# Kernel optimization log

Hardware: AMD Instinct MI355X
Metric: run time of the kernel (lower is better)

Reference implementation:

```python
import jax, jax.numpy as jnp
import numpy as np

E, H, FF = 1024, 16, 4096
HD = E // H
B, S = 4, 2048


def _ln(x, g, b, eps=1e-5):
    m = jnp.mean(x, axis=-1, keepdims=True)
    v = jnp.mean((x - m) ** 2, axis=-1, keepdims=True)
    return (x - m) / jnp.sqrt(v + eps) * g + b


def setup_inputs() -> dict:
    k = jax.random.key(0)
    ks = jax.random.split(k, 12)
    sd = 0.02
    return {
        "value": jax.random.normal(ks[0], (B, S, E), jnp.float32),
        "key": jax.random.normal(ks[1], (B, S, E), jnp.float32),
        "query": jax.random.normal(ks[2], (B, S, E), jnp.float32),
        "mask": jnp.ones((B, 1, 1, S), jnp.int32),
        "Wv": sd * jax.random.normal(ks[3], (E, E), jnp.float32),
        "Wk": sd * jax.random.normal(ks[4], (E, E), jnp.float32),
        "Wq": sd * jax.random.normal(ks[5], (E, E), jnp.float32),
        "Wo": sd * jax.random.normal(ks[6], (E, E), jnp.float32),
        "bo": jnp.zeros((E,), jnp.float32),
        "ln1_g": jnp.ones((E,), jnp.float32), "ln1_b": jnp.zeros((E,), jnp.float32),
        "ln2_g": jnp.ones((E,), jnp.float32), "ln2_b": jnp.zeros((E,), jnp.float32),
        "lnf_g": jnp.ones((E,), jnp.float32), "lnf_b": jnp.zeros((E,), jnp.float32),
        "W1": sd * jax.random.normal(ks[7], (E, FF), jnp.float32),
        "b1": jnp.zeros((FF,), jnp.float32),
        "W2": sd * jax.random.normal(ks[8], (FF, E), jnp.float32),
        "b2": jnp.zeros((E,), jnp.float32),
    }


def reference(value, key, query, mask, Wv, Wk, Wq, Wo, bo,
              ln1_g, ln1_b, ln2_g, ln2_b, lnf_g, lnf_b, W1, b1, W2, b2):
    N, Sq, Em = query.shape
    # pre-norms (value & key share prenorm2 params, as in the torch module)
    v = _ln(value, ln2_g, ln2_b)
    k = _ln(key, ln2_g, ln2_b)
    q = _ln(query, ln1_g, ln1_b)
    # QKV projections (no bias), split heads
    V = (v @ Wv).reshape(N, v.shape[1], H, HD)
    K = (k @ Wk).reshape(N, k.shape[1], H, HD)
    Q = (q @ Wq).reshape(N, Sq, H, HD)
    energy = jnp.einsum("nqhd,nkhd->nhqk", Q, K)  # [N,H,Sq,Sk]
    energy = jnp.where(mask == 0, jnp.float32(-1e20), energy)
    attn = jax.nn.softmax(energy / jnp.float32(HD ** 0.5), axis=-1)
    out = jnp.einsum("nhqk,nkhd->nqhd", attn, V).reshape(N, Sq, Em)
    out = out @ Wo + bo
    x = out + q  # residual (drop_path is identity in eval)
    f = _ln(x, lnf_g, lnf_b) @ W1 + b1
    f = jax.nn.gelu(f, approximate=False) @ W2 + b2
    return f + x
```

## Files before the change

kernel.cpp:

```cpp
#include <hip/hip_runtime.h>
#include <hip/hip_bf16.h>
#include <math.h>

typedef __bf16 bf16x8 __attribute__((ext_vector_type(8)));
typedef __bf16 bf16x4 __attribute__((ext_vector_type(4)));
typedef float f32x4 __attribute__((ext_vector_type(4)));
typedef float f32x2 __attribute__((ext_vector_type(2)));
typedef short s16x4 __attribute__((ext_vector_type(4)));

#define AS1 __attribute__((address_space(1)))
#define AS3 __attribute__((address_space(3)))

__device__ __forceinline__ void gll16(const __bf16* g, __bf16* l) {
    __builtin_amdgcn_global_load_lds((const AS1 unsigned int*)g,
                                     (AS3 unsigned int*)l, 16, 0, 0);
}

#if __has_builtin(__builtin_amdgcn_exp2f)
#define EXP2(x) __builtin_amdgcn_exp2f(x)
#else
#define EXP2(x) __expf((x) * 0.69314718055994530942f)
#endif

__device__ __forceinline__ f32x4 mfma16x16(bf16x4 a, bf16x4 b, f32x4 c) {
#if __has_builtin(__builtin_amdgcn_mfma_f32_16x16x16bf16_1k)
    union { bf16x4 h; s16x4 s; } ua, ub;
    ua.h = a; ub.h = b;
    return __builtin_amdgcn_mfma_f32_16x16x16bf16_1k(ua.s, ub.s, c, 0, 0, 0);
#else
    f32x4 d = c;
    asm volatile("v_mfma_f32_16x16x16_bf16 %0, %1, %2, %0"
                 : "+v"(d) : "v"(a), "v"(b));
    return d;
#endif
}

__global__ __launch_bounds__(256) void transpose_all(
    const float* __restrict__ Wq, const float* __restrict__ Wk,
    const float* __restrict__ Wv, const float* __restrict__ Wo,
    const float* __restrict__ W1, const float* __restrict__ W2,
    __bf16* __restrict__ Wqt, __bf16* __restrict__ Wkt,
    __bf16* __restrict__ Wvt, __bf16* __restrict__ Wot,
    __bf16* __restrict__ W1t, __bf16* __restrict__ W2t) {
    int g = blockIdx.x;
    const float* W; __bf16* Wt; int K, N, kt, nt;
    if (g < 4096) {
        int mi = g >> 10, loc = g & 1023;
        K = 1024; N = 1024; kt = loc >> 5; nt = loc & 31;
        W  = mi == 0 ? Wq  : mi == 1 ? Wk  : mi == 2 ? Wv  : Wo;
        Wt = mi == 0 ? Wqt : mi == 1 ? Wkt : mi == 2 ? Wvt : Wot;
    } else if (g < 8192) {
        int loc = g - 4096; W = W1; Wt = W1t;
        K = 1024; N = 4096; kt = loc >> 7; nt = loc & 127;
    } else {
        int loc = g - 8192; W = W2; Wt = W2t;
        K = 4096; N = 1024; kt = loc >> 5; nt = loc & 31;
    }
    int k0 = kt * 32, n0 = nt * 32;
    __shared__ float tile[32][33];
    int tx = threadIdx.x & 31, ty = threadIdx.x >> 5;
    #pragma unroll
    for (int j = ty; j < 32; j += 8)
        tile[j][tx] = W[(size_t)(k0 + j) * N + n0 + tx];
    __syncthreads();
    #pragma unroll
    for (int j = ty; j < 32; j += 8)
        Wt[(size_t)(n0 + j) * K + k0 + tx] = (__bf16)tile[tx][j];
}

__global__ __launch_bounds__(256) void ln3_kernel(
    const float* __restrict__ q, const float* __restrict__ k,
    const float* __restrict__ v,
    const float* __restrict__ g1, const float* __restrict__ b1,
    const float* __restrict__ g2, const float* __restrict__ b2,
    float* __restrict__ qln, __bf16* __restrict__ qbf,
    __bf16* __restrict__ kbf, __bf16* __restrict__ vbf) {
    const int E = 1024;
    int which = blockIdx.y;
    const float* x = which == 0 ? q : which == 1 ? k : v;
    const float* g = which == 0 ? g1 : g2;
    const float* bb = which == 0 ? b1 : b2;
    float* o32 = which == 0 ? qln : nullptr;
    __bf16* obf = which == 0 ? qbf : which == 1 ? kbf : vbf;

    size_t row = blockIdx.x;
    int t = threadIdx.x;
    float4 val = ((const float4*)(x + row * E))[t];
    float s  = val.x + val.y + val.z + val.w;
    float s2 = val.x * val.x + val.y * val.y + val.z * val.z + val.w * val.w;
    #pragma unroll
    for (int off = 32; off >= 1; off >>= 1) {
        s  += __shfl_down(s, off);
        s2 += __shfl_down(s2, off);
    }
    __shared__ float red[2][4];
    int wid = t >> 6, lane = t & 63;
    if (lane == 0) { red[0][wid] = s; red[1][wid] = s2; }
    __syncthreads();
    if (t == 0) {
        float S1 = red[0][0] + red[0][1] + red[0][2] + red[0][3];
        float S2 = red[1][0] + red[1][1] + red[1][2] + red[1][3];
        float mean = S1 / E;
        float var  = S2 / E - mean * mean;
        red[0][0] = mean;
        red[1][0] = 1.0f / sqrtf(var + 1e-5f);
    }
    __syncthreads();
    float mean = red[0][0], rstd = red[1][0];
    float4 gv = ((const float4*)g)[t];
    float4 bv = ((const float4*)bb)[t];
    float y0 = (val.x - mean) * rstd * gv.x + bv.x;
    float y1 = (val.y - mean) * rstd * gv.y + bv.y;
    float y2 = (val.z - mean) * rstd * gv.z + bv.z;
    float y3 = (val.w - mean) * rstd * gv.w + bv.w;
    if (o32) ((float4*)(o32 + row * E))[t] = make_float4(y0, y1, y2, y3);
    bf16x4 o;
    o[0] = (__bf16)y0; o[1] = (__bf16)y1; o[2] = (__bf16)y2; o[3] = (__bf16)y3;
    ((bf16x4*)(obf + row * E))[t] = o;
}

__global__ __launch_bounds__(256) void ln_kernel(const float* __restrict__ x,
                                                 const float* __restrict__ g,
                                                 const float* __restrict__ bb,
                                                 __bf16* __restrict__ outbf) {
    const int E = 1024;
    size_t row = blockIdx.x;
    int t = threadIdx.x;
    float4 v = ((const float4*)(x + row * E))[t];
    float s  = v.x + v.y + v.z + v.w;
    float s2 = v.x * v.x + v.y * v.y + v.z * v.z + v.w * v.w;
    #pragma unroll
    for (int off = 32; off >= 1; off >>= 1) {
        s  += __shfl_down(s, off);
        s2 += __shfl_down(s2, off);
    }
    __shared__ float red[2][4];
    int wid = t >> 6, lane = t & 63;
    if (lane == 0) { red[0][wid] = s; red[1][wid] = s2; }
    __syncthreads();
    if (t == 0) {
        float S1 = red[0][0] + red[0][1] + red[0][2] + red[0][3];
        float S2 = red[1][0] + red[1][1] + red[1][2] + red[1][3];
        float mean = S1 / E;
        float var  = S2 / E - mean * mean;
        red[0][0] = mean;
        red[1][0] = 1.0f / sqrtf(var + 1e-5f);
    }
    __syncthreads();
    float mean = red[0][0], rstd = red[1][0];
    float4 gv = ((const float4*)g)[t];
    float4 bv = ((const float4*)bb)[t];
    bf16x4 o;
    o[0] = (__bf16)((v.x - mean) * rstd * gv.x + bv.x);
    o[1] = (__bf16)((v.y - mean) * rstd * gv.y + bv.y);
    o[2] = (__bf16)((v.z - mean) * rstd * gv.z + bv.z);
    o[3] = (__bf16)((v.w - mean) * rstd * gv.w + bv.w);
    ((bf16x4*)(outbf + row * E))[t] = o;
}

template <int EPI>
__global__ __launch_bounds__(256) void gemm128(const __bf16* __restrict__ A,
                                               const __bf16* __restrict__ A2,
                                               const __bf16* __restrict__ Bt,
                                               const __bf16* __restrict__ Bt2,
                                               const float* __restrict__ bias,
                                               const float* __restrict__ resid,
                                               void* __restrict__ Cout,
                                               int M, int N, int K,
                                               int splitN, float scale) {
    __shared__ __bf16 As[128 * 64];
    __shared__ __bf16 Bs[128 * 64];
    int tid  = threadIdx.x;
    int lane = tid & 63, wid = tid >> 6;
    int quad = lane >> 4, l15 = lane & 15;
    int waveM = wid >> 1, waveN = wid & 1;

    int GX = N >> 7;
    int id = blockIdx.x;
    int x8 = id & 7, t = id >> 3;
    size_t rowBase = (size_t)((t / GX) * 8 + x8) * 128;
    size_t colBase = (size_t)(t % GX) * 128;

    const __bf16* Ap = A; const __bf16* Bp = Bt;
    size_t colLoc = colBase;
    float sc = scale;
    if ((int)colBase >= splitN) { Ap = A2; Bp = Bt2; colLoc = colBase - splitN; sc = 1.0f; }

    int lrow8  = lane >> 3;
    int lchunk = (lane & 7) ^ lrow8;
    const __bf16* Ag0 = Ap + (rowBase + wid * 32 + lrow8) * (size_t)K + lchunk * 8;
    const __bf16* Bg0 = Bp + (colLoc  + wid * 32 + lrow8) * (size_t)K + lchunk * 8;
    __bf16* AsB = &As[(wid * 32) * 64];
    __bf16* BsB = &Bs[(wid * 32) * 64];

    f32x4 acc[4][4] = {};
    int swz = l15 & 7;

    for (int kb = 0; kb < K; kb += 64) {
        __syncthreads();
        #pragma unroll
        for (int i = 0; i < 4; i++) {
            gll16(Ag0 + (size_t)i * 8 * K + kb, AsB + i * 512);
            gll16(Bg0 + (size_t)i * 8 * K + kb, BsB + i * 512);
        }
        __syncthreads();
        #pragma unroll
        for (int ks = 0; ks < 2; ks++) {
            int p = ((ks * 4 + quad) ^ swz) * 8;
            bf16x8 af[4], bfr[4];
            #pragma unroll
            for (int mi = 0; mi < 4; mi++)
                af[mi] = *(const bf16x8*)&As[(waveM * 64 + mi * 16 + l15) * 64 + p];
            #pragma unroll
            for (int ni = 0; ni < 4; ni++)
                bfr[ni] = *(const bf16x8*)&Bs[(waveN * 64 + ni * 16 + l15) * 64 + p];
            #pragma unroll
            for (int mi = 0; mi < 4; mi++)
                #pragma unroll
                for (int ni = 0; ni < 4; ni++)
                    acc[mi][ni] = __builtin_amdgcn_mfma_f32_16x16x32_bf16(
                        bfr[ni], af[mi], acc[mi][ni], 0, 0, 0);
        }
    }

    #pragma unroll
    for (int mi = 0; mi < 4; mi++)
    #pragma unroll
    for (int ni = 0; ni < 4; ni++) {
        size_t row = rowBase + waveM * 64 + mi * 16 + l15;
        size_t col = colBase + waveN * 64 + ni * 16 + quad * 4;
        f32x4 v = acc[mi][ni];
        if (EPI == 1) {
            float4 b4 = *(const float4*)&bias[col];
            float4 r4 = *(const float4*)&resid[row * N + col];
            float4 o;
            o.x = v[0] + b4.x + r4.x; o.y = v[1] + b4.y + r4.y;
            o.z = v[2] + b4.z + r4.z; o.w = v[3] + b4.w + r4.w;
            *(float4*)&((float*)Cout)[row * N + col] = o;
        } else if (EPI == 2) {
            float4 b4 = *(const float4*)&bias[col];
            bf16x4 pk;
            #pragma unroll
            for (int r = 0; r < 4; r++) {
                float t2 = v[r] + ((const float*)&b4)[r];
                pk[r] = (__bf16)(0.5f * t2 * (1.0f + erff(t2 * 0.70710678118654752f)));
            }
            *(bf16x4*)&((__bf16*)Cout)[row * N + col] = pk;
        } else {
            bf16x4 pk;
            #pragma unroll
            for (int r = 0; r < 4; r++) pk[r] = (__bf16)(v[r] * sc);
            *(bf16x4*)&((__bf16*)Cout)[row * N + col] = pk;
        }
    }
}

__global__ __launch_bounds__(256) void gemmV(const __bf16* __restrict__ A,
                                             const __bf16* __restrict__ Bt,
                                             __bf16* __restrict__ Cout,
                                             int M, int N, int K) {
    __shared__ __bf16 As[128 * 64];
    __shared__ __bf16 Bs[128 * 64];
    int tid  = threadIdx.x;
    int lane = tid & 63, wid = tid >> 6;
    int quad = lane >> 4, l15 = lane & 15;
    int waveM = wid >> 1, waveN = wid & 1;

    int GX = N >> 7;
    int id = blockIdx.x;
    int x8 = id & 7, t = id >> 3;
    size_t rowBase = (size_t)((t / GX) * 8 + x8) * 128;
    size_t colBase = (size_t)(t % GX) * 128;

    int lrow8  = lane >> 3;
    int lchunk = (lane & 7) ^ lrow8;
    const __bf16* Ag0 = A  + (rowBase + wid * 32 + lrow8) * (size_t)K + lchunk * 8;
    const __bf16* Bg0 = Bt + (colBase + wid * 32 + lrow8) * (size_t)K + lchunk * 8;
    __bf16* AsB = &As[(wid * 32) * 64];
    __bf16* BsB = &Bs[(wid * 32) * 64];

    f32x4 acc[4][4] = {};
    int swz = l15 & 7;

    for (int kb = 0; kb < K; kb += 64) {
        __syncthreads();
        #pragma unroll
        for (int i = 0; i < 4; i++) {
            gll16(Ag0 + (size_t)i * 8 * K + kb, AsB + i * 512);
            gll16(Bg0 + (size_t)i * 8 * K + kb, BsB + i * 512);
        }
        __syncthreads();
        #pragma unroll
        for (int ks = 0; ks < 2; ks++) {
            int p = ((ks * 4 + quad) ^ swz) * 8;
            bf16x8 af[4], bfr[4];
            #pragma unroll
            for (int mi = 0; mi < 4; mi++)
                af[mi] = *(const bf16x8*)&As[(waveM * 64 + mi * 16 + l15) * 64 + p];
            #pragma unroll
            for (int ni = 0; ni < 4; ni++)
                bfr[ni] = *(const bf16x8*)&Bs[(waveN * 64 + ni * 16 + l15) * 64 + p];
            #pragma unroll
            for (int mi = 0; mi < 4; mi++)
                #pragma unroll
                for (int ni = 0; ni < 4; ni++)
                    acc[mi][ni] = __builtin_amdgcn_mfma_f32_16x16x32_bf16(
                        af[mi], bfr[ni], acc[mi][ni], 0, 0, 0);
        }
    }

    #pragma unroll
    for (int mi = 0; mi < 4; mi++)
    #pragma unroll
    for (int ni = 0; ni < 4; ni++) {
        size_t col = colBase + waveN * 64 + ni * 16 + l15;
        size_t m0  = rowBase + waveM * 64 + mi * 16 + quad * 4;
        bf16x4 pk;
        #pragma unroll
        for (int r = 0; r < 4; r++) pk[r] = (__bf16)acc[mi][ni][r];
        *(bf16x4*)&Cout[col * M + m0] = pk;
    }
}

__global__ __launch_bounds__(512, 4) void attn_kernel(const __bf16* __restrict__ QK,
                                                      const __bf16* __restrict__ Vt,
                                                      const int* __restrict__ mask,
                                                      __bf16* __restrict__ Out) {
    const int S = 2048, E = 1024, E2 = 2048, M = 8192;
    int qt = blockIdx.x, bh = blockIdx.y;
    int b = bh >> 4, h = bh & 15;
    int q0 = qt * 256;
    int tid = threadIdx.x, lane = tid & 63, wid = tid >> 6;
    int quad = lane >> 4, l15 = lane & 15;

    __shared__ __bf16 Ks[2][4096];
    __shared__ __bf16 Vs[2][4096];

    bf16x8 aq[2][2];
    #pragma unroll
    for (int g = 0; g < 2; g++)
    #pragma unroll
    for (int hh = 0; hh < 2; hh++) {
        size_t row = (size_t)(b * S + q0 + wid * 32 + g * 16 + l15);
        aq[g][hh] = *(const bf16x8*)(QK + row * E2 + h * 64 + hh * 32 + quad * 8);
    }

    int lrow8  = lane >> 3;
    int lchunk = (lane & 7) ^ lrow8;
    const __bf16* Kg0 = QK + (size_t)(b * S + wid * 8 + lrow8) * E2 + 1024 + h * 64 + lchunk * 8;

    int rv = tid >> 3, cv = tid & 7;
    const __bf16* Vg0 = Vt + (size_t)(h * 64 + rv) * M + b * S + cv * 8;
    int c0   = ((cv & 1) << 2) + (cv >> 2);
    int lowb = (cv >> 1) & 1;
    int sv   = rv & 7;
    int wo0  = rv * 64 + ((c0 ^ sv) << 3) + (lowb << 2);
    int wo1  = rv * 64 + (((c0 + 2) ^ sv) << 3) + (lowb << 2);

    int swz = l15 & 7;

    f32x4 accO[2][4] = {};
    f32x2 acc2[2] = {};

    bf16x8 vreg = *(const bf16x8*)(Vg0);
    gll16(Kg0, &Ks[0][wid * 512]);
    *(bf16x4*)&Vs[0][wo0] = __builtin_shufflevector(vreg, vreg, 0, 1, 2, 3);
    *(bf16x4*)&Vs[0][wo1] = __builtin_shufflevector(vreg, vreg, 4, 5, 6, 7);
    __syncthreads();

    for (int kt = 0; kt < S / 64; kt++) {
        int k0 = kt * 64;
        int buf = kt & 1;
        if (kt + 1 < S / 64) {
            vreg = *(const bf16x8*)(Vg0 + k0 + 64);
            gll16(Kg0 + (size_t)(k0 + 64) * E2, &Ks[buf ^ 1][wid * 512]);
        }
        const __bf16* Ksb = &Ks[buf][0];
        const __bf16* Vsb = &Vs[buf][0];

        bf16x4 pb[2][4];
        #pragma unroll
        for (int nt = 0; nt < 4; nt++) {
            bf16x8 a0 = *(const bf16x8*)&Ksb[(nt * 16 + l15) * 64 + ((quad) ^ swz) * 8];
            bf16x8 a1 = *(const bf16x8*)&Ksb[(nt * 16 + l15) * 64 + ((4 + quad) ^ swz) * 8];
            int4 mz = *(const int4*)&mask[b * S + k0 + nt * 16 + quad * 4];
            #pragma unroll
            for (int g = 0; g < 2; g++) {
                f32x4 a = {};
                a = __builtin_amdgcn_mfma_f32_16x16x32_bf16(a0, aq[g][0], a, 0, 0, 0);
                a = __builtin_amdgcn_mfma_f32_16x16x32_bf16(a1, aq[g][1], a, 0, 0, 0);
                float p0 = mz.x ? EXP2(a[0]) : 0.f;
                float p1 = mz.y ? EXP2(a[1]) : 0.f;
                float p2 = mz.z ? EXP2(a[2]) : 0.f;
                float p3 = mz.w ? EXP2(a[3]) : 0.f;
                f32x2 t01; t01[0] = p0; t01[1] = p1;
                f32x2 t23; t23[0] = p2; t23[1] = p3;
                acc2[g] += t01 + t23;
                bf16x4 pk;
                pk[0] = (__bf16)p0; pk[1] = (__bf16)p1;
                pk[2] = (__bf16)p2; pk[3] = (__bf16)p3;
                pb[g][nt] = pk;
            }
        }

        #pragma unroll
        for (int dt = 0; dt < 4; dt++) {
            const __bf16* vrow = &Vsb[(dt * 16 + l15) * 64];
            bf16x8 vv0 = *(const bf16x8*)&vrow[((quad * 2 + 0) ^ swz) * 8];
            bf16x8 vv1 = *(const bf16x8*)&vrow[((quad * 2 + 1) ^ swz) * 8];
            bf16x4 h00 = __builtin_shufflevector(vv0, vv0, 0, 1, 2, 3);
            bf16x4 h01 = __builtin_shufflevector(vv0, vv0, 4, 5, 6, 7);
            bf16x4 h10 = __builtin_shufflevector(vv1, vv1, 0, 1, 2, 3);
            bf16x4 h11 = __builtin_shufflevector(vv1, vv1, 4, 5, 6, 7);
            #pragma unroll
            for (int g = 0; g < 2; g++) {
                accO[g][dt] = mfma16x16(h00, pb[g][0], accO[g][dt]);
                accO[g][dt] = mfma16x16(h01, pb[g][1], accO[g][dt]);
                accO[g][dt] = mfma16x16(h10, pb[g][2], accO[g][dt]);
                accO[g][dt] = mfma16x16(h11, pb[g][3], accO[g][dt]);
            }
        }

        if (kt + 1 < S / 64) {
            *(bf16x4*)&Vs[buf ^ 1][wo0] = __builtin_shufflevector(vreg, vreg, 0, 1, 2, 3);
            *(bf16x4*)&Vs[buf ^ 1][wo1] = __builtin_shufflevector(vreg, vreg, 4, 5, 6, 7);
        }
        __syncthreads();
    }

    #pragma unroll
    for (int g = 0; g < 2; g++) {
        float l = acc2[g][0] + acc2[g][1];
        l += __shfl_xor(l, 16, 64);
        l += __shfl_xor(l, 32, 64);
        float inv = 1.0f / l;
        #pragma unroll
        for (int dt = 0; dt < 4; dt++) {
            size_t row = (size_t)(b * S + q0 + wid * 32 + g * 16 + l15);
            bf16x4 pk;
            #pragma unroll
            for (int r = 0; r < 4; r++) pk[r] = (__bf16)(accO[g][dt][r] * inv);
            *(bf16x4*)&Out[row * E + h * 64 + dt * 16 + quad * 4] = pk;
        }
    }
}

extern "C" void kernel_launch(void* const* d_in, const int* in_sizes, int n_in,
                              void* d_out, int out_size, void* d_ws, size_t ws_size,
                              hipStream_t stream) {
    const int Bb = 4, S = 2048, E = 1024, FF = 4096;
    const int M = Bb * S;

    const float* value = (const float*)d_in[0];
    const float* key   = (const float*)d_in[1];
    const float* query = (const float*)d_in[2];
    const int*   mask  = (const int*)d_in[3];
    const float* Wv    = (const float*)d_in[4];
    const float* Wk    = (const float*)d_in[5];
    const float* Wq    = (const float*)d_in[6];
    const float* Wo    = (const float*)d_in[7];
    const float* bo    = (const float*)d_in[8];
    const float* ln1_g = (const float*)d_in[9];
    const float* ln1_b = (const float*)d_in[10];
    const float* ln2_g = (const float*)d_in[11];
    const float* ln2_b = (const float*)d_in[12];
    const float* lnf_g = (const float*)d_in[13];
    const float* lnf_b = (const float*)d_in[14];
    const float* W1    = (const float*)d_in[15];
    const float* b1    = (const float*)d_in[16];
    const float* W2    = (const float*)d_in[17];
    const float* b2    = (const float*)d_in[18];

    char* ws = (char*)d_ws;
    const size_t MB = 1024 * 1024;
    __bf16* Wqt = (__bf16*)(ws + 0 * MB);
    __bf16* Wkt = (__bf16*)(ws + 2 * MB);
    __bf16* Wvt = (__bf16*)(ws + 4 * MB);
    __bf16* Wot = (__bf16*)(ws + 6 * MB);
    __bf16* W1t = (__bf16*)(ws + 8 * MB);
    __bf16* W2t = (__bf16*)(ws + 16 * MB);
    __bf16* q_bf = (__bf16*)(ws + 24 * MB);
    __bf16* k_bf = (__bf16*)(ws + 40 * MB);
    __bf16* v_bf = (__bf16*)(ws + 56 * MB);
    __bf16* QKb  = (__bf16*)(ws + 72 * MB);
    __bf16* Vtg  = (__bf16*)(ws + 104 * MB);
    __bf16* attn = q_bf;
    __bf16* x_ln = k_bf;
    __bf16* h1   = v_bf;
    float*  qln  = (float*)(ws + 120 * MB);
    float*  x32  = (float*)(ws + 152 * MB);

    transpose_all<<<12288, 256, 0, stream>>>(Wq, Wk, Wv, Wo, W1, W2,
                                             Wqt, Wkt, Wvt, Wot, W1t, W2t);

    ln3_kernel<<<dim3(M, 3), 256, 0, stream>>>(query, key, value,
                                               ln1_g, ln1_b, ln2_g, ln2_b,
                                               qln, q_bf, k_bf, v_bf);

    gemm128<0><<<16 * 64, 256, 0, stream>>>(
        q_bf, k_bf, Wqt, Wkt, nullptr, nullptr, QKb, M, 2 * E, E, E,
        0.125f * 1.44269504088896f);

    gemmV<<<8 * 64, 256, 0, stream>>>(v_bf, Wvt, Vtg, M, E, E);

    attn_kernel<<<dim3(S / 256, Bb * 16), 512, 0, stream>>>(QKb, Vtg, mask, attn);

    gemm128<1><<<8 * 64, 256, 0, stream>>>(
        attn, attn, Wot, Wot, bo, qln, x32, M, E, E, E, 1.0f);

    ln_kernel<<<M, 256, 0, stream>>>(x32, lnf_g, lnf_b, x_ln);

    gemm128<2><<<32 * 64, 256, 0, stream>>>(
        x_ln, x_ln, W1t, W1t, b1, nullptr, h1, M, FF, E, FF, 1.0f);
    gemm128<1><<<8 * 64, 256, 0, stream>>>(
        h1, h1, W2t, W2t, b2, x32, (float*)d_out, M, E, FF, E, 1.0f);
}
```

Before: 652.9 us.

## Add 256x256 double-buffered GEMM kernel for QK projection and FFN1

Introduces a gemm256 kernel with 256x256 output tiles, 512 threads (8 waves), LDS double buffering via global_load_lds, and interleaved MFMA phases with s_setprio to overlap loads with compute. It replaces gemm128 for the fused Q/K projection and the W1+GELU GEMM. Larger tiles raise arithmetic intensity and cut global traffic per FLOP. In exchange, LDS use grows to 128KB per block and there are fewer blocks (256 for QK), which may underfill the CUs.

```diff
diff --git a/kernel.cpp b/kernel.cpp
--- a/kernel.cpp
+++ b/kernel.cpp
@@ -255,6 +255,168 @@
     }
 }
 
+template <int EPI>
+__global__ __launch_bounds__(512, 2) void gemm256(const __bf16* __restrict__ A,
+                                                  const __bf16* __restrict__ A2,
+                                                  const __bf16* __restrict__ Bt,
+                                                  const __bf16* __restrict__ Bt2,
+                                                  const float* __restrict__ bias,
+                                                  const float* __restrict__ resid,
+                                                  void* __restrict__ Cout,
+                                                  int M, int N, int K,
+                                                  int splitN, float scale) {
+    __shared__ __bf16 As[2][256 * 64];
+    __shared__ __bf16 Bs[2][256 * 64];
+    int tid  = threadIdx.x;
+    int lane = tid & 63, wid = tid >> 6;
+    int quad = lane >> 4, l15 = lane & 15;
+    int waveM = wid >> 2, waveN = wid & 3;
+
+    int GX = N >> 8;
+    int id = blockIdx.x;
+    int x8 = id & 7, tt = id >> 3;
+    size_t rowBase = (size_t)((tt / GX) * 8 + x8) * 256;
+    size_t colBase = (size_t)(tt % GX) * 256;
+
+    const __bf16* Ap = A; const __bf16* Bp = Bt;
+    size_t colLoc = colBase;
+    float sc = scale;
+    if ((int)colBase >= splitN) { Ap = A2; Bp = Bt2; colLoc = colBase - splitN; sc = 1.0f; }
+
+    int lrow8  = lane >> 3;
+    int lchunk = (lane & 7) ^ lrow8;
+    const __bf16* Ag0 = Ap + (rowBase + wid * 32 + lrow8) * (size_t)K + lchunk * 8;
+    const __bf16* Bg0 = Bp + (colLoc  + wid * 32 + lrow8) * (size_t)K + lchunk * 8;
+    int ldsB = (wid * 32) * 64;
+
+    f32x4 acc[8][4] = {};
+    int swz = l15 & 7;
+    int nsteps = K >> 6;
+
+    #pragma unroll
+    for (int i = 0; i < 4; i++) {
+        gll16(Ag0 + (size_t)i * 8 * K, &As[0][ldsB + i * 512]);
+        gll16(Bg0 + (size_t)i * 8 * K, &Bs[0][ldsB + i * 512]);
+    }
+    __syncthreads();
+
+    for (int t = 0; t < nsteps; t++) {
+        int cur = t & 1;
+        const __bf16* Asb = &As[cur][0];
+        const __bf16* Bsb = &Bs[cur][0];
+        __bf16* Asn = &As[cur ^ 1][0];
+        __bf16* Bsn = &Bs[cur ^ 1][0];
+        bool pre = (t + 1 < nsteps);
+        size_t kb = (size_t)(t + 1) << 6;
+
+        bf16x8 af[4], bfr[4];
+        int p0 = (quad ^ swz) * 8;
+        int p1 = ((4 + quad) ^ swz) * 8;
+
+        #pragma unroll
+        for (int ni = 0; ni < 4; ni++)
+            bfr[ni] = *(const bf16x8*)&Bsb[(waveN * 64 + ni * 16 + l15) * 64 + p0];
+        #pragma unroll
+        for (int mi = 0; mi < 4; mi++)
+            af[mi] = *(const bf16x8*)&Asb[(waveM * 128 + mi * 16 + l15) * 64 + p0];
+        if (pre) {
+            #pragma unroll
+            for (int i = 0; i < 4; i++)
+                gll16(Ag0 + (size_t)i * 8 * K + kb, &Asn[ldsB + i * 512]);
+        }
+        __builtin_amdgcn_s_barrier();
+        __builtin_amdgcn_s_setprio(1);
+        #pragma unroll
+        for (int mi = 0; mi < 4; mi++)
+            #pragma unroll
+            for (int ni = 0; ni < 4; ni++)
+                acc[mi][ni] = __builtin_amdgcn_mfma_f32_16x16x32_bf16(
+                    bfr[ni], af[mi], acc[mi][ni], 0, 0, 0);
+        __builtin_amdgcn_s_setprio(0);
+        __builtin_amdgcn_s_barrier();
+
+        #pragma unroll
+        for (int mi = 0; mi < 4; mi++)
+            af[mi] = *(const bf16x8*)&Asb[(waveM * 128 + (mi + 4) * 16 + l15) * 64 + p0];
+        if (pre) {
+            #pragma unroll
+            for (int i = 0; i < 4; i++)
+                gll16(Bg0 + (size_t)i * 8 * K + kb, &Bsn[ldsB + i * 512]);
+        }
+        __builtin_amdgcn_s_barrier();
+        __builtin_amdgcn_s_setprio(1);
+        #pragma unroll
+        for (int mi = 0; mi < 4; mi++)
+            #pragma unroll
+            for (int ni = 0; ni < 4; ni++)
+                acc[mi + 4][ni] = __builtin_amdgcn_mfma_f32_16x16x32_bf16(
+                    bfr[ni], af[mi], acc[mi + 4][ni], 0, 0, 0);
+        __builtin_amdgcn_s_setprio(0);
+        __builtin_amdgcn_s_barrier();
+
+        #pragma unroll
+        for (int ni = 0; ni < 4; ni++)
+            bfr[ni] = *(const bf16x8*)&Bsb[(waveN * 64 + ni * 16 + l15) * 64 + p1];
+        #pragma unroll
+        for (int mi = 0; mi < 4; mi++)
+            af[mi] = *(const bf16x8*)&Asb[(waveM * 128 + mi * 16 + l15) * 64 + p1];
+        __builtin_amdgcn_s_barrier();
+        __builtin_amdgcn_s_setprio(1);
+        #pragma unroll
+        for (int mi = 0; mi < 4; mi++)
+            #pragma unroll
+            for (int ni = 0; ni < 4; ni++)
+                acc[mi][ni] = __builtin_amdgcn_mfma_f32_16x16x32_bf16(
+                    bfr[ni], af[mi], acc[mi][ni], 0, 0, 0);
+        __builtin_amdgcn_s_setprio(0);
+        __builtin_amdgcn_s_barrier();
+
+        #pragma unroll
+        for (int mi = 0; mi < 4; mi++)
+            af[mi] = *(const bf16x8*)&Asb[(waveM * 128 + (mi + 4) * 16 + l15) * 64 + p1];
+        __builtin_amdgcn_s_setprio(1);
+        #pragma unroll
+        for (int mi = 0; mi < 4; mi++)
+            #pragma unroll
+            for (int ni = 0; ni < 4; ni++)
+                acc[mi + 4][ni] = __builtin_amdgcn_mfma_f32_16x16x32_bf16(
+                    bfr[ni], af[mi], acc[mi + 4][ni], 0, 0, 0);
+        __builtin_amdgcn_s_setprio(0);
+        __syncthreads();
+    }
+
+    #pragma unroll
+    for (int mi = 0; mi < 8; mi++)
+    #pragma unroll
+    for (int ni = 0; ni < 4; ni++) {
+        size_t row = rowBase + waveM * 128 + mi * 16 + l15;
+        size_t col = colBase + waveN * 64 + ni * 16 + quad * 4;
+        f32x4 v = acc[mi][ni];
+        if (EPI == 1) {
+            float4 b4 = *(const float4*)&bias[col];
+            float4 r4 = *(const float4*)&resid[row * N + col];
+            float4 o;
+            o.x = v[0] + b4.x + r4.x; o.y = v[1] + b4.y + r4.y;
+            o.z = v[2] + b4.z + r4.z; o.w = v[3] + b4.w + r4.w;
+            *(float4*)&((float*)Cout)[row * N + col] = o;
+        } else if (EPI == 2) {
+            float4 b4 = *(const float4*)&bias[col];
+            bf16x4 pk;
+            #pragma unroll
+            for (int r = 0; r < 4; r++) {
+                float t2 = v[r] + ((const float*)&b4)[r];
+                pk[r] = (__bf16)(0.5f * t2 * (1.0f + erff(t2 * 0.70710678118654752f)));
+            }
+            *(bf16x4*)&((__bf16*)Cout)[row * N + col] = pk;
+        } else {
+            bf16x4 pk;
+            #pragma unroll
+            for (int r = 0; r < 4; r++) pk[r] = (__bf16)(v[r] * sc);
+            *(bf16x4*)&((__bf16*)Cout)[row * N + col] = pk;
+        }
+    }
+}
+
 __global__ __launch_bounds__(256) void gemmV(const __bf16* __restrict__ A,
                                              const __bf16* __restrict__ Bt,
                                              __bf16* __restrict__ Cout,
@@ -497,7 +659,7 @@
                                                ln1_g, ln1_b, ln2_g, ln2_b,
                                                qln, q_bf, k_bf, v_bf);
 
-    gemm128<0><<<16 * 64, 256, 0, stream>>>(
+    gemm256<0><<<256, 512, 0, stream>>>(
         q_bf, k_bf, Wqt, Wkt, nullptr, nullptr, QKb, M, 2 * E, E, E,
         0.125f * 1.44269504088896f);
 
@@ -510,7 +672,7 @@
 
     ln_kernel<<<M, 256, 0, stream>>>(x32, lnf_g, lnf_b, x_ln);
 
-    gemm128<2><<<32 * 64, 256, 0, stream>>>(
+    gemm256<2><<<512, 512, 0, stream>>>(
         x_ln, x_ln, W1t, W1t, b1, nullptr, h1, M, FF, E, FF, 1.0f);
     gemm128<1><<<8 * 64, 256, 0, stream>>>(
         h1, h1, W2t, W2t, b2, x32, (float*)d_out, M, E, FF, E, 1.0f);
```

Result: faster. 623.9 us (-4.4%).

## Replace GEMM with triple-buffered 256x128 tile kernel using async LDS loads

Applied to the files above, without the earlier changes.

The 128x128 single-buffer GEMM is replaced with a 256x128-tile kernel using 512 threads. Its LDS ring holds three buffers filled by global_load_lds. The next tiles are prefetched two k-steps ahead and gated by explicit vmcnt waits and raw s_barrier calls, with s_setprio raised around the MFMA blocks. This aims to hide global-load latency behind matrix math and raise per-block data reuse. In exchange it uses about 144KB of LDS per block, which allows fewer resident blocks, and the hand-written wait counts must match the number of loads in flight.

```diff
diff --git a/kernel.cpp b/kernel.cpp
--- a/kernel.cpp
+++ b/kernel.cpp
@@ -15,6 +15,8 @@
     __builtin_amdgcn_global_load_lds((const AS1 unsigned int*)g,
                                      (AS3 unsigned int*)l, 16, 0, 0);
 }
+
+#define VMCNT(n) asm volatile("s_waitcnt vmcnt(" #n ")" ::: "memory")
 
 #if __has_builtin(__builtin_amdgcn_exp2f)
 #define EXP2(x) __builtin_amdgcn_exp2f(x)
@@ -159,17 +161,17 @@
 }
 
 template <int EPI>
-__global__ __launch_bounds__(256) void gemm128(const __bf16* __restrict__ A,
-                                               const __bf16* __restrict__ A2,
-                                               const __bf16* __restrict__ Bt,
-                                               const __bf16* __restrict__ Bt2,
-                                               const float* __restrict__ bias,
-                                               const float* __restrict__ resid,
-                                               void* __restrict__ Cout,
-                                               int M, int N, int K,
-                                               int splitN, float scale) {
-    __shared__ __bf16 As[128 * 64];
-    __shared__ __bf16 Bs[128 * 64];
+__global__ __launch_bounds__(512, 2) void gemm256x128(const __bf16* __restrict__ A,
+                                                      const __bf16* __restrict__ A2,
+                                                      const __bf16* __restrict__ Bt,
+                                                      const __bf16* __restrict__ Bt2,
+                                                      const float* __restrict__ bias,
+                                                      const float* __restrict__ resid,
+                                                      void* __restrict__ Cout,
+                                                      int M, int N, int K,
+                                                      int splitN, float scale) {
+    __shared__ __bf16 As[3][256 * 64];
+    __shared__ __bf16 Bs[3][128 * 64];
     int tid  = threadIdx.x;
     int lane = tid & 63, wid = tid >> 6;
     int quad = lane >> 4, l15 = lane & 15;
@@ -177,9 +179,9 @@
 
     int GX = N >> 7;
     int id = blockIdx.x;
-    int x8 = id & 7, t = id >> 3;
-    size_t rowBase = (size_t)((t / GX) * 8 + x8) * 128;
-    size_t colBase = (size_t)(t % GX) * 128;
+    int x8 = id & 7, tt = id >> 3;
+    size_t rowBase = (size_t)((tt / GX) * 8 + x8) * 256;
+    size_t colBase = (size_t)(tt % GX) * 128;
 
     const __bf16* Ap = A; const __bf16* Bp = Bt;
     size_t colLoc = colBase;
@@ -189,39 +191,78 @@
     int lrow8  = lane >> 3;
     int lchunk = (lane & 7) ^ lrow8;
     const __bf16* Ag0 = Ap + (rowBase + wid * 32 + lrow8) * (size_t)K + lchunk * 8;
-    const __bf16* Bg0 = Bp + (colLoc  + wid * 32 + lrow8) * (size_t)K + lchunk * 8;
-    __bf16* AsB = &As[(wid * 32) * 64];
-    __bf16* BsB = &Bs[(wid * 32) * 64];
+    const __bf16* Bg0 = Bp + (colLoc  + wid * 16 + lrow8) * (size_t)K + lchunk * 8;
+    int ldsA = (wid * 32) * 64;
+    int ldsB = (wid * 16) * 64;
+
+#define STAGE_A4(buf, kt) { _Pragma("unroll") \
+    for (int i = 0; i < 4; i++) \
+        gll16(Ag0 + (size_t)i * 8 * K + (size_t)(kt) * 64, &As[buf][ldsA + i * 512]); }
+#define STAGE_B2(buf, kt) { _Pragma("unroll") \
+    for (int i = 0; i < 2; i++) \
+        gll16(Bg0 + (size_t)i * 8 * K + (size_t)(kt) * 64, &Bs[buf][ldsB + i * 512]); }
 
     f32x4 acc[4][4] = {};
     int swz = l15 & 7;
-
-    for (int kb = 0; kb < K; kb += 64) {
-        __syncthreads();
-        #pragma unroll
-        for (int i = 0; i < 4; i++) {
-            gll16(Ag0 + (size_t)i * 8 * K + kb, AsB + i * 512);
-            gll16(Bg0 + (size_t)i * 8 * K + kb, BsB + i * 512);
-        }
-        __syncthreads();
-        #pragma unroll
-        for (int ks = 0; ks < 2; ks++) {
-            int p = ((ks * 4 + quad) ^ swz) * 8;
-            bf16x8 af[4], bfr[4];
-            #pragma unroll
-            for (int mi = 0; mi < 4; mi++)
-                af[mi] = *(const bf16x8*)&As[(waveM * 64 + mi * 16 + l15) * 64 + p];
+    int nsteps = K >> 6;
+
+    STAGE_A4(0, 0); STAGE_B2(0, 0);
+    STAGE_A4(1, 1); STAGE_B2(1, 1);
+    VMCNT(6);
+    __builtin_amdgcn_s_barrier();
+
+    bf16x8 af[4], bfr[4];
+    int p0 = (quad ^ swz) * 8;
+    int p1 = ((4 + quad) ^ swz) * 8;
+
+    int cb = 0;
+    for (int T = 0; T < nsteps; T++) {
+        int nb = cb + 2; if (nb >= 3) nb -= 3;
+        int S = T + 2 < nsteps ? T + 2 : nsteps - 1;
+        const __bf16* Asb = &As[cb][0];
+        const __bf16* Bsb = &Bs[cb][0];
+
+        #pragma unroll
+        for (int ni = 0; ni < 4; ni++)
+            bfr[ni] = *(const bf16x8*)&Bsb[(waveN * 64 + ni * 16 + l15) * 64 + p0];
+        #pragma unroll
+        for (int mi = 0; mi < 4; mi++)
+            af[mi] = *(const bf16x8*)&Asb[(waveM * 64 + mi * 16 + l15) * 64 + p0];
+        STAGE_A4(nb, S);
+        __builtin_amdgcn_s_barrier();
+        __builtin_amdgcn_s_setprio(1);
+        #pragma unroll
+        for (int mi = 0; mi < 4; mi++)
             #pragma unroll
             for (int ni = 0; ni < 4; ni++)
-                bfr[ni] = *(const bf16x8*)&Bs[(waveN * 64 + ni * 16 + l15) * 64 + p];
-            #pragma unroll
-            for (int mi = 0; mi < 4; mi++)
-                #pragma unroll
-                for (int ni = 0; ni < 4; ni++)
-                    acc[mi][ni] = __builtin_amdgcn_mfma_f32_16x16x32_bf16(
-                        bfr[ni], af[mi], acc[mi][ni], 0, 0, 0);
-        }
-    }
+                acc[mi][ni] = __builtin_amdgcn_mfma_f32_16x16x32_bf16(
+                    bfr[ni], af[mi], acc[mi][ni], 0, 0, 0);
+        __builtin_amdgcn_s_setprio(0);
+        __builtin_amdgcn_s_barrier();
+
+        #pragma unroll
+        for (int ni = 0; ni < 4; ni++)
+            bfr[ni] = *(const bf16x8*)&Bsb[(waveN * 64 + ni * 16 + l15) * 64 + p1];
+        #pragma unroll
+        for (int mi = 0; mi < 4; mi++)
+            af[mi] = *(const bf16x8*)&Asb[(waveM * 64 + mi * 16 + l15) * 64 + p1];
+        STAGE_B2(nb, S);
+        VMCNT(6);
+        __builtin_amdgcn_s_barrier();
+        __builtin_amdgcn_s_setprio(1);
+        #pragma unroll
+        for (int mi = 0; mi < 4; mi++)
+            #pragma unroll
+            for (int ni = 0; ni < 4; ni++)
+                acc[mi][ni] = __builtin_amdgcn_mfma_f32_16x16x32_bf16(
+                    bfr[ni], af[mi], acc[mi][ni], 0, 0, 0);
+        __builtin_amdgcn_s_setprio(0);
+        __builtin_amdgcn_s_barrier();
+
+        cb = cb + 1 == 3 ? 0 : cb + 1;
+    }
+#undef STAGE_A4
+#undef STAGE_B2
 
     #pragma unroll
     for (int mi = 0; mi < 4; mi++)
@@ -497,7 +538,7 @@
                                                ln1_g, ln1_b, ln2_g, ln2_b,
                                                qln, q_bf, k_bf, v_bf);
 
-    gemm128<0><<<16 * 64, 256, 0, stream>>>(
+    gemm256x128<0><<<512, 512, 0, stream>>>(
         q_bf, k_bf, Wqt, Wkt, nullptr, nullptr, QKb, M, 2 * E, E, E,
         0.125f * 1.44269504088896f);
 
@@ -505,13 +546,13 @@
 
     attn_kernel<<<dim3(S / 256, Bb * 16), 512, 0, stream>>>(QKb, Vtg, mask, attn);
 
-    gemm128<1><<<8 * 64, 256, 0, stream>>>(
+    gemm256x128<1><<<256, 512, 0, stream>>>(
         attn, attn, Wot, Wot, bo, qln, x32, M, E, E, E, 1.0f);
 
     ln_kernel<<<M, 256, 0, stream>>>(x32, lnf_g, lnf_b, x_ln);
 
-    gemm128<2><<<32 * 64, 256, 0, stream>>>(
+    gemm256x128<2><<<1024, 512, 0, stream>>>(
         x_ln, x_ln, W1t, W1t, b1, nullptr, h1, M, FF, E, FF, 1.0f);
-    gemm128<1><<<8 * 64, 256, 0, stream>>>(
+    gemm256x128<1><<<256, 512, 0, stream>>>(
         h1, h1, W2t, W2t, b2, x32, (float*)d_out, M, E, FF, E, 1.0f);
 }
```

New measurement: 639.6 us. 1.02x faster.
